# Performance work log

Measured on AMD Instinct MI355X. Metric: run time of the kernel, lower is better.

## Reference

```python
import jax, jax.numpy as jnp
from jax import lax
import numpy as np

# inferred ssconv semantics (custom CUDA kernel not in source):
#  - input x: (B, H, W, Cin) channels-last, Cin = per-pixel channel count
#  - in_index: (B, H, W) in [0, IN_GROUPS): routes each input pixel's Cin channels
#    to the corresponding slice of the weight's input-channel dim (gather/scatter MoE-style dispatch)
#  - weight: (OUT_GROUPS*Cout, IN_GROUPS*Cin, kh, kw), bias: (OUT_GROUPS*Cout,)
#  - per output pixel, one out-group is selected (maxout over groups); the kernel
#    returns both the selected Cout channels and the winning group index (out_index)

IN_GROUPS = 4
OUT_GROUPS = 4
STRIDE = 1  # pad = stride//2 in the wrapper; output (H-1)//s+1 == SAME padding


def setup_inputs() -> dict:
    key = jax.random.key(0)
    k1, k2, k3, k4 = jax.random.split(key, 4)
    x = jax.random.normal(k1, (8, 256, 256, 16), dtype=jnp.float32)
    in_index = jax.random.randint(k2, (8, 256, 256), 0, IN_GROUPS, dtype=jnp.int32)
    weight = jax.random.normal(k3, (64, 64, 3, 3), dtype=jnp.float32) * 0.05
    bias = jax.random.normal(k4, (64,), dtype=jnp.float32) * 0.05
    return {"x": x, "in_index": in_index, "weight": weight, "bias": bias}


def reference(x, in_index, weight, bias):
    B, H, W, Cin = x.shape
    OC, IC, kh, kw = weight.shape  # OC = OUT_GROUPS*Cout, IC = IN_GROUPS*Cin
    Cout = OC // OUT_GROUPS

    # dispatch: scatter each pixel's channels into its in-group slice (rest zero)
    onehot = jax.nn.one_hot(in_index, IN_GROUPS, dtype=x.dtype)          # (B,H,W,G)
    x_full = (onehot[..., :, None] * x[..., None, :]).reshape(B, H, W, IN_GROUPS * Cin)

    # dense conv over the dispatched tensor == per-pixel gathered group weights
    w_hwio = jnp.transpose(weight, (2, 3, 1, 0))  # (kh,kw,IC,OC)
    out = lax.conv_general_dilated(
        x_full, w_hwio, window_strides=(STRIDE, STRIDE), padding="SAME",
        dimension_numbers=("NHWC", "HWIO", "NHWC"))
    out = out + bias  # (B,H',W',OC)

    Bo, Ho, Wo, _ = out.shape
    out_g = out.reshape(Bo, Ho, Wo, OUT_GROUPS, Cout)
    scores = out_g.max(axis=-1)                    # (B,H',W',G) per-group response
    out_index = jnp.argmax(scores, axis=-1)        # winning out-group per pixel
    sel = jnp.take_along_axis(out_g, out_index[..., None, None], axis=3)
    sel = jnp.squeeze(sel, axis=3)                 # (B,H',W',Cout)
    return sel, out_index.astype(jnp.int32)
```

## Files before the change

kernel.cpp:

```cpp
#include <hip/hip_runtime.h>

#define H 256
#define W 256
#define BATCH 8
#define CIN 16
#define TW 32
#define TH 4
#define HWC (TW + 2)
#define HHC (TH + 2)
#define NHALO (HWC * HHC)
#define PXB 80
#define FIX_CAP 16384
#define GAP_TAU 2e-3f

#define OFF_XF   16384
#define XF_TERM  (NHALO * PXB)
#define OFF_SW   49024
#define OFF_BIAS 49280
#define OFF_RED  49536
#define SMEM_BYTES 49552

typedef __attribute__((ext_vector_type(4))) int i32x4;

__device__ __forceinline__ void gload_lds16(const void* g, void* l) {
    __builtin_amdgcn_global_load_lds(
        (const __attribute__((address_space(1))) unsigned int*)g,
        (__attribute__((address_space(3))) unsigned int*)l, 16, 0, 0);
}

template <int CTRL>
__device__ __forceinline__ float dpp_maxstep(float v) {
    int t = __builtin_amdgcn_update_dpp(0, __float_as_int(v), CTRL, 0xF, 0xF, true);
    return fmaxf(v, __int_as_float(t));
}
__device__ __forceinline__ float rowmax16(float v) {
    v = dpp_maxstep<0xB1>(v);
    v = dpp_maxstep<0x4E>(v);
    v = dpp_maxstep<0x124>(v);
    v = dpp_maxstep<0x128>(v);
    return v;
}

__global__ void wprep_kernel(const float* __restrict__ w, char* __restrict__ wt,
                             float* __restrict__ sw_ws, unsigned* __restrict__ fix_cnt) {
    const int n = blockIdx.x;
    const int k = threadIdx.x;
    if (n == 0 && k == 0) fix_cnt[0] = 0u;

    float v[9];
    float m = 0.f;
#pragma unroll
    for (int t = 0; t < 9; ++t) {
        v[t] = w[(n * 64 + k) * 9 + t];
        m = fmaxf(m, fabsf(v[t]));
    }
#pragma unroll
    for (int s = 1; s < 64; s <<= 1) m = fmaxf(m, __shfl_xor(m, s, 64));
    const float inv = (m > 0.f) ? (127.f / m) : 0.f;
    if (k == 0) sw_ws[n] = m * (1.f / 127.f);

    const int nt = n >> 4, nl = n & 15, kq = k >> 4, j = k & 15;
    const int lane16 = (kq * 16 + nl) * 16 + j;
#pragma unroll
    for (int t = 0; t < 9; ++t) {
        float f = v[t] * inv;
        int h = __float2int_rn(f);
        int l = __float2int_rn((f - (float)h) * 128.f);
        wt[((t * 2 + 0) * 4 + nt) * 1024 + lane16] = (char)h;
        wt[((t * 2 + 1) * 4 + nt) * 1024 + lane16] = (char)l;
    }
}

__global__ __launch_bounds__(256, 3) void ssconv_i8_kernel(
    const float* __restrict__ x, const int* __restrict__ gidx,
    const char* __restrict__ wt, const float* __restrict__ sw_ws,
    const float* __restrict__ bias,
    float* __restrict__ out_sel, float* __restrict__ out_idx,
    unsigned* __restrict__ fix_cnt, unsigned* __restrict__ fix_list)
{
    __shared__ __align__(16) char smem[SMEM_BYTES];
    char*  bufB  = smem;
    char*  xF    = smem + OFF_XF;
    float* swdL  = (float*)(smem + OFF_SW);
    float* biasL = (float*)(smem + OFF_BIAS);
    float* redL  = (float*)(smem + OFF_RED);

    const int tid  = threadIdx.x;
    const int x0   = blockIdx.x * TW;
    const int y0   = blockIdx.y * TH;
    const int bz   = blockIdx.z;
    const int wvid = tid >> 6;
    const int L    = tid & 63;
    const int q    = L >> 4;
    const int lm   = L & 15;

#pragma unroll
    for (int it = 0; it < 2; ++it) {
        int seg = it * 4 + wvid;
        gload_lds16(wt + seg * 1024 + L * 16, bufB + seg * 1024 + L * 16);
    }

    if (tid < 64) { swdL[tid] = sw_ws[tid]; biasL[tid] = bias[tid]; }

    float4 av0 = make_float4(0, 0, 0, 0), av1 = av0, av2 = av0, av3 = av0;
    int gv = 0;
    float am = 0.f;
    if (tid < NHALO) {
        int r = tid / HWC, c = tid - r * HWC;
        int hy = y0 + r - 1, hx = x0 + c - 1;
        if (hy >= 0 && hy < H && hx >= 0 && hx < W) {
            const float4* src = (const float4*)(x + (((size_t)bz * H + hy) * W + hx) * CIN);
            av0 = src[0]; av1 = src[1]; av2 = src[2]; av3 = src[3];
            gv = gidx[((size_t)bz * H + hy) * W + hx];
        }
        am = fmaxf(fmaxf(fmaxf(fabsf(av0.x), fabsf(av0.y)), fmaxf(fabsf(av0.z), fabsf(av0.w))),
              fmaxf(fmaxf(fmaxf(fabsf(av1.x), fabsf(av1.y)), fmaxf(fabsf(av1.z), fabsf(av1.w))),
              fmaxf(fmaxf(fmaxf(fabsf(av2.x), fabsf(av2.y)), fmaxf(fabsf(av2.z), fabsf(av2.w))),
                    fmaxf(fmaxf(fabsf(av3.x), fabsf(av3.y)), fmaxf(fabsf(av3.z), fabsf(av3.w))))));
    }
#pragma unroll
    for (int s = 1; s < 64; s <<= 1) am = fmaxf(am, __shfl_xor(am, s, 64));
    if (L == 0) redL[wvid] = am;
    __syncthreads();
    float bm = fmaxf(fmaxf(redL[0], redL[1]), fmaxf(redL[2], redL[3]));
    const float qinv = (bm > 0.f) ? (127.f / bm) : 0.f;
    const float sB   = bm * (1.f / 127.f);

    if (tid < NHALO) {
        float fs[16] = {av0.x, av0.y, av0.z, av0.w, av1.x, av1.y, av1.z, av1.w,
                        av2.x, av2.y, av2.z, av2.w, av3.x, av3.y, av3.z, av3.w};
        unsigned hw[4], lw[4];
#pragma unroll
        for (int j = 0; j < 4; ++j) {
            unsigned hword = 0, lword = 0;
#pragma unroll
            for (int e = 0; e < 4; ++e) {
                float f_ = fs[j * 4 + e] * qinv;
                int h_ = __float2int_rn(f_);
                int l_ = __float2int_rn((f_ - (float)h_) * 128.f);
                hword |= ((unsigned)(h_ & 255)) << (8 * e);
                lword |= ((unsigned)(l_ & 255)) << (8 * e);
            }
            hw[j] = hword; lw[j] = lword;
        }
        uint4 zz = make_uint4(0, 0, 0, 0);
        char* ph = xF + tid * PXB;
        char* pl = xF + XF_TERM + tid * PXB;
#pragma unroll
        for (int s = 0; s < 4; ++s) {
            *(uint4*)(ph + s * 16) = (s == gv) ? make_uint4(hw[0], hw[1], hw[2], hw[3]) : zz;
            *(uint4*)(pl + s * 16) = (s == gv) ? make_uint4(lw[0], lw[1], lw[2], lw[3]) : zz;
        }
    }
    __syncthreads();

    i32x4 acc1[2][4] = {};
    i32x4 acc2[2][4] = {};

#pragma unroll 1
    for (int tap = 0; tap < 9; ++tap) {
        if (tap < 8) {
            const char* gsrc = wt + (size_t)(tap + 1) * 8192;
            char* ldst = bufB + ((tap + 1) & 1) * 8192;
#pragma unroll
            for (int it = 0; it < 2; ++it) {
                int seg = it * 4 + wvid;
                gload_lds16(gsrc + seg * 1024 + L * 16, ldst + seg * 1024 + L * 16);
            }
        }

        const char* bB = bufB + (tap & 1) * 8192;
        const int dy = tap / 3, dx = tap - dy * 3;
        const int hbase = (wvid + dy) * HWC + lm + dx;

        i32x4 bh[4], bl[4];
#pragma unroll
        for (int nt = 0; nt < 4; ++nt) {
            bh[nt] = *(const i32x4*)(bB + nt * 1024 + L * 16);
            bl[nt] = *(const i32x4*)(bB + 4096 + nt * 1024 + L * 16);
        }
#pragma unroll
        for (int m = 0; m < 2; ++m) {
            const char* pA = xF + (hbase + 16 * m) * PXB + q * 16;
            i32x4 a0 = *(const i32x4*)pA;
            i32x4 a1 = *(const i32x4*)(pA + XF_TERM);
#pragma unroll
            for (int nt = 0; nt < 4; ++nt) {
                acc1[m][nt] = __builtin_amdgcn_mfma_i32_16x16x64_i8(a0, bh[nt], acc1[m][nt], 0, 0, 0);
                acc2[m][nt] = __builtin_amdgcn_mfma_i32_16x16x64_i8(a0, bl[nt], acc2[m][nt], 0, 0, 0);
                acc2[m][nt] = __builtin_amdgcn_mfma_i32_16x16x64_i8(a1, bh[nt], acc2[m][nt], 0, 0, 0);
            }
        }
        __syncthreads();
    }

    float swb[4], bsr[4];
#pragma unroll
    for (int nt = 0; nt < 4; ++nt) {
        swb[nt] = sB * swdL[nt * 16 + lm];
        bsr[nt] = biasL[nt * 16 + lm];
    }

    const int gy = y0 + wvid;
#pragma unroll
    for (int m = 0; m < 2; ++m) {
#pragma unroll
        for (int r = 0; r < 4; ++r) {
            float v0 = swb[0] * ((float)acc1[m][0][r] + (float)acc2[m][0][r] * (1.f / 128.f)) + bsr[0];
            float v1 = swb[1] * ((float)acc1[m][1][r] + (float)acc2[m][1][r] * (1.f / 128.f)) + bsr[1];
            float v2 = swb[2] * ((float)acc1[m][2][r] + (float)acc2[m][2][r] * (1.f / 128.f)) + bsr[2];
            float v3 = swb[3] * ((float)acc1[m][3][r] + (float)acc2[m][3][r] * (1.f / 128.f)) + bsr[3];

            float g0 = rowmax16(v0);
            float g1 = rowmax16(v1);
            float g2 = rowmax16(v2);
            float g3 = rowmax16(v3);
            int bg = 0; float best = g0;
            if (g1 > best) { best = g1; bg = 1; }
            if (g2 > best) { best = g2; bg = 2; }
            if (g3 > best) { best = g3; bg = 3; }

            float selv = (bg == 0) ? v0 : (bg == 1) ? v1 : (bg == 2) ? v2 : v3;

            const int gx = x0 + m * 16 + q * 4 + r;
            const size_t opix = ((size_t)bz * H + gy) * W + gx;
            out_sel[opix * 16 + lm] = selv;

            if (lm == 0) {
                out_idx[opix] = (float)bg;
                float o1v = (bg == 0) ? g1 : g0;
                float o2v = (bg <= 1) ? g2 : g1;
                float o3v = (bg <= 2) ? g3 : g2;
                float second = fmaxf(o1v, fmaxf(o2v, o3v));
                if (best - second < GAP_TAU) {
                    unsigned slot = atomicAdd(fix_cnt, 1u);
                    if (slot < FIX_CAP) fix_list[slot] = (unsigned)opix;
                }
            }
        }
    }
}

__global__ void fixup_kernel(const float* __restrict__ x, const int* __restrict__ gidx,
                             const float* __restrict__ w, const float* __restrict__ bias,
                             float* __restrict__ out_sel, float* __restrict__ out_idx,
                             const unsigned* __restrict__ fix_cnt,
                             const unsigned* __restrict__ fix_list)
{
    unsigned n = *fix_cnt;
    if (n > FIX_CAP) n = FIX_CAP;
    const int lane = threadIdx.x & 63;
    const int nwaves = gridDim.x * (blockDim.x >> 6);
    unsigned widx = blockIdx.x * (blockDim.x >> 6) + (threadIdx.x >> 6);

    for (; widx < n; widx += nwaves) {
        unsigned opix = fix_list[widx];
        int b  = opix >> 16;
        int y  = (opix >> 8) & 255;
        int xc = opix & 255;
        double acc = (double)bias[lane];
        for (int dy = 0; dy < 3; ++dy) {
            int yy = y + dy - 1;
            if (yy < 0 || yy >= H) continue;
            for (int dx = 0; dx < 3; ++dx) {
                int xx = xc + dx - 1;
                if (xx < 0 || xx >= W) continue;
                size_t pix = ((size_t)b * H + yy) * W + xx;
                int g = gidx[pix];
                const float* xp = x + pix * 16;
                const float* wp = w + (size_t)(lane * 64 + g * 16) * 9 + (dy * 3 + dx);
#pragma unroll
                for (int c = 0; c < 16; ++c)
                    acc = fma((double)wp[c * 9], (double)xp[c], acc);
            }
        }
        double m = acc;
        m = fmax(m, __shfl_xor(m, 1, 64));
        m = fmax(m, __shfl_xor(m, 2, 64));
        m = fmax(m, __shfl_xor(m, 4, 64));
        m = fmax(m, __shfl_xor(m, 8, 64));
        double g0 = __shfl(m, 0, 64), g1 = __shfl(m, 16, 64);
        double g2 = __shfl(m, 32, 64), g3 = __shfl(m, 48, 64);
        int bg = 0; double bb = g0;
        if (g1 > bb) { bb = g1; bg = 1; }
        if (g2 > bb) { bb = g2; bg = 2; }
        if (g3 > bb) { bb = g3; bg = 3; }
        if ((lane >> 4) == bg) out_sel[(size_t)opix * 16 + (lane & 15)] = (float)acc;
        if (lane == 0) out_idx[opix] = (float)bg;
    }
}

extern "C" void kernel_launch(void* const* d_in, const int* in_sizes, int n_in,
                              void* d_out, int out_size, void* d_ws, size_t ws_size,
                              hipStream_t stream) {
    const float* x    = (const float*)d_in[0];
    const int*   gidx = (const int*)d_in[1];
    const float* w    = (const float*)d_in[2];
    const float* bias = (const float*)d_in[3];

    char*     wt       = (char*)d_ws;
    float*    sw_ws    = (float*)((char*)d_ws + 73728);
    unsigned* fix_cnt  = (unsigned*)((char*)d_ws + 73984);
    unsigned* fix_list = (unsigned*)((char*)d_ws + 74000);

    float* out_sel = (float*)d_out;
    float* out_idx = (float*)d_out + (size_t)BATCH * H * W * CIN;

    wprep_kernel<<<64, 64, 0, stream>>>(w, wt, sw_ws, fix_cnt);

    dim3 grid(W / TW, H / TH, BATCH);
    ssconv_i8_kernel<<<grid, 256, 0, stream>>>(x, gidx, wt, sw_ws, bias,
                                               out_sel, out_idx, fix_cnt, fix_list);
    fixup_kernel<<<256, 256, 0, stream>>>(x, gidx, w, bias, out_sel, out_idx,
                                          fix_cnt, fix_list);
}
```

Before: 215.8 us.

## Replace split-int8 MFMA conv with fp16 MFMA and on-the-fly group masking

```diff
diff --git a/kernel.cpp b/kernel.cpp
--- a/kernel.cpp
+++ b/kernel.cpp
@@ -9,18 +9,23 @@
 #define HWC (TW + 2)
 #define HHC (TH + 2)
 #define NHALO (HWC * HHC)
-#define PXB 80
+#define PXA 40
 #define FIX_CAP 16384
-#define GAP_TAU 2e-3f
-
-#define OFF_XF   16384
-#define XF_TERM  (NHALO * PXB)
-#define OFF_SW   49024
-#define OFF_BIAS 49280
-#define OFF_RED  49536
-#define SMEM_BYTES 49552
-
-typedef __attribute__((ext_vector_type(4))) int i32x4;
+#define GAP_TAU 6e-3f
+
+#define OFF_XH   16384
+#define OFF_GS   24544
+#define OFF_BIAS 25360
+#define SMEM_BYTES 25616
+
+typedef __attribute__((ext_vector_type(8))) short short8;
+typedef __attribute__((ext_vector_type(8))) _Float16 half8;
+typedef __attribute__((ext_vector_type(4))) float f32x4;
+
+union S8H8 { short8 s; half8 h; };
+__device__ __forceinline__ half8 as_h8(short8 s) { S8H8 u; u.s = s; return u.h; }
+union HU { _Float16 h; unsigned short u; };
+__device__ __forceinline__ unsigned short f2h(float f) { HU u; u.h = (_Float16)f; return u.u; }
 
 __device__ __forceinline__ void gload_lds16(const void* g, void* l) {
     __builtin_amdgcn_global_load_lds(
@@ -41,49 +46,31 @@
     return v;
 }
 
-__global__ void wprep_kernel(const float* __restrict__ w, char* __restrict__ wt,
-                             float* __restrict__ sw_ws, unsigned* __restrict__ fix_cnt) {
+__global__ void wprep_kernel(const float* __restrict__ w, unsigned short* __restrict__ wt,
+                             unsigned* __restrict__ fix_cnt) {
     const int n = blockIdx.x;
     const int k = threadIdx.x;
     if (n == 0 && k == 0) fix_cnt[0] = 0u;
 
-    float v[9];
-    float m = 0.f;
-#pragma unroll
-    for (int t = 0; t < 9; ++t) {
-        v[t] = w[(n * 64 + k) * 9 + t];
-        m = fmaxf(m, fabsf(v[t]));
-    }
-#pragma unroll
-    for (int s = 1; s < 64; s <<= 1) m = fmaxf(m, __shfl_xor(m, s, 64));
-    const float inv = (m > 0.f) ? (127.f / m) : 0.f;
-    if (k == 0) sw_ws[n] = m * (1.f / 127.f);
-
-    const int nt = n >> 4, nl = n & 15, kq = k >> 4, j = k & 15;
-    const int lane16 = (kq * 16 + nl) * 16 + j;
-#pragma unroll
-    for (int t = 0; t < 9; ++t) {
-        float f = v[t] * inv;
-        int h = __float2int_rn(f);
-        int l = __float2int_rn((f - (float)h) * 128.f);
-        wt[((t * 2 + 0) * 4 + nt) * 1024 + lane16] = (char)h;
-        wt[((t * 2 + 1) * 4 + nt) * 1024 + lane16] = (char)l;
-    }
-}
-
-__global__ __launch_bounds__(256, 3) void ssconv_i8_kernel(
+    const int nt = n >> 4, lm = n & 15;
+    const int ks = k >> 5, q = (k >> 3) & 3, j = k & 7;
+    const int dst = ((0 * 2 + ks) * 4 + nt) * 512 + (q * 16 + lm) * 8 + j;
+#pragma unroll
+    for (int t = 0; t < 9; ++t)
+        wt[dst + t * 4096] = f2h(w[(n * 64 + k) * 9 + t] * 64.0f);
+}
+
+__global__ __launch_bounds__(256, 4) void ssconv_f16_kernel(
     const float* __restrict__ x, const int* __restrict__ gidx,
-    const char* __restrict__ wt, const float* __restrict__ sw_ws,
-    const float* __restrict__ bias,
+    const unsigned short* __restrict__ wt, const float* __restrict__ bias,
     float* __restrict__ out_sel, float* __restrict__ out_idx,
     unsigned* __restrict__ fix_cnt, unsigned* __restrict__ fix_list)
 {
     __shared__ __align__(16) char smem[SMEM_BYTES];
     char*  bufB  = smem;
-    char*  xF    = smem + OFF_XF;
-    float* swdL  = (float*)(smem + OFF_SW);
+    char*  xH    = smem + OFF_XH;
+    int*   gsL   = (int*)(smem + OFF_GS);
     float* biasL = (float*)(smem + OFF_BIAS);
-    float* redL  = (float*)(smem + OFF_RED);
 
     const int tid  = threadIdx.x;
     const int x0   = blockIdx.x * TW;
@@ -93,74 +80,43 @@
     const int L    = tid & 63;
     const int q    = L >> 4;
     const int lm   = L & 15;
+    const int c0   = (q & 1) * 8;
 
 #pragma unroll
     for (int it = 0; it < 2; ++it) {
         int seg = it * 4 + wvid;
-        gload_lds16(wt + seg * 1024 + L * 16, bufB + seg * 1024 + L * 16);
-    }
-
-    if (tid < 64) { swdL[tid] = sw_ws[tid]; biasL[tid] = bias[tid]; }
-
-    float4 av0 = make_float4(0, 0, 0, 0), av1 = av0, av2 = av0, av3 = av0;
-    int gv = 0;
-    float am = 0.f;
+        gload_lds16((const char*)wt + seg * 1024 + L * 16, bufB + seg * 1024 + L * 16);
+    }
+
+    if (tid < 64) biasL[tid] = bias[tid];
+
     if (tid < NHALO) {
         int r = tid / HWC, c = tid - r * HWC;
         int hy = y0 + r - 1, hx = x0 + c - 1;
+        float4 a0 = make_float4(0, 0, 0, 0), a1 = a0, a2 = a0, a3 = a0;
+        int g = 0;
         if (hy >= 0 && hy < H && hx >= 0 && hx < W) {
             const float4* src = (const float4*)(x + (((size_t)bz * H + hy) * W + hx) * CIN);
-            av0 = src[0]; av1 = src[1]; av2 = src[2]; av3 = src[3];
-            gv = gidx[((size_t)bz * H + hy) * W + hx];
-        }
-        am = fmaxf(fmaxf(fmaxf(fabsf(av0.x), fabsf(av0.y)), fmaxf(fabsf(av0.z), fabsf(av0.w))),
-              fmaxf(fmaxf(fmaxf(fabsf(av1.x), fabsf(av1.y)), fmaxf(fabsf(av1.z), fabsf(av1.w))),
-              fmaxf(fmaxf(fmaxf(fabsf(av2.x), fabsf(av2.y)), fmaxf(fabsf(av2.z), fabsf(av2.w))),
-                    fmaxf(fmaxf(fabsf(av3.x), fabsf(av3.y)), fmaxf(fabsf(av3.z), fabsf(av3.w))))));
-    }
-#pragma unroll
-    for (int s = 1; s < 64; s <<= 1) am = fmaxf(am, __shfl_xor(am, s, 64));
-    if (L == 0) redL[wvid] = am;
+            a0 = src[0]; a1 = src[1]; a2 = src[2]; a3 = src[3];
+            g = gidx[((size_t)bz * H + hy) * W + hx];
+        }
+        short8 v0, v1;
+        v0[0] = (short)f2h(a0.x); v0[1] = (short)f2h(a0.y); v0[2] = (short)f2h(a0.z); v0[3] = (short)f2h(a0.w);
+        v0[4] = (short)f2h(a1.x); v0[5] = (short)f2h(a1.y); v0[6] = (short)f2h(a1.z); v0[7] = (short)f2h(a1.w);
+        v1[0] = (short)f2h(a2.x); v1[1] = (short)f2h(a2.y); v1[2] = (short)f2h(a2.z); v1[3] = (short)f2h(a2.w);
+        v1[4] = (short)f2h(a3.x); v1[5] = (short)f2h(a3.y); v1[6] = (short)f2h(a3.z); v1[7] = (short)f2h(a3.w);
+        *(short8*)(xH + tid * PXA + 0)  = v0;
+        *(short8*)(xH + tid * PXA + 16) = v1;
+        gsL[tid] = g;
+    }
     __syncthreads();
-    float bm = fmaxf(fmaxf(redL[0], redL[1]), fmaxf(redL[2], redL[3]));
-    const float qinv = (bm > 0.f) ? (127.f / bm) : 0.f;
-    const float sB   = bm * (1.f / 127.f);
-
-    if (tid < NHALO) {
-        float fs[16] = {av0.x, av0.y, av0.z, av0.w, av1.x, av1.y, av1.z, av1.w,
-                        av2.x, av2.y, av2.z, av2.w, av3.x, av3.y, av3.z, av3.w};
-        unsigned hw[4], lw[4];
-#pragma unroll
-        for (int j = 0; j < 4; ++j) {
-            unsigned hword = 0, lword = 0;
-#pragma unroll
-            for (int e = 0; e < 4; ++e) {
-                float f_ = fs[j * 4 + e] * qinv;
-                int h_ = __float2int_rn(f_);
-                int l_ = __float2int_rn((f_ - (float)h_) * 128.f);
-                hword |= ((unsigned)(h_ & 255)) << (8 * e);
-                lword |= ((unsigned)(l_ & 255)) << (8 * e);
-            }
-            hw[j] = hword; lw[j] = lword;
-        }
-        uint4 zz = make_uint4(0, 0, 0, 0);
-        char* ph = xF + tid * PXB;
-        char* pl = xF + XF_TERM + tid * PXB;
-#pragma unroll
-        for (int s = 0; s < 4; ++s) {
-            *(uint4*)(ph + s * 16) = (s == gv) ? make_uint4(hw[0], hw[1], hw[2], hw[3]) : zz;
-            *(uint4*)(pl + s * 16) = (s == gv) ? make_uint4(lw[0], lw[1], lw[2], lw[3]) : zz;
-        }
-    }
-    __syncthreads();
-
-    i32x4 acc1[2][4] = {};
-    i32x4 acc2[2][4] = {};
+
+    f32x4 acc[2][4] = {};
 
 #pragma unroll 1
     for (int tap = 0; tap < 9; ++tap) {
         if (tap < 8) {
-            const char* gsrc = wt + (size_t)(tap + 1) * 8192;
+            const char* gsrc = (const char*)wt + (size_t)(tap + 1) * 8192;
             char* ldst = bufB + ((tap + 1) & 1) * 8192;
 #pragma unroll
             for (int it = 0; it < 2; ++it) {
@@ -173,43 +129,49 @@
         const int dy = tap / 3, dx = tap - dy * 3;
         const int hbase = (wvid + dy) * HWC + lm + dx;
 
-        i32x4 bh[4], bl[4];
-#pragma unroll
-        for (int nt = 0; nt < 4; ++nt) {
-            bh[nt] = *(const i32x4*)(bB + nt * 1024 + L * 16);
-            bl[nt] = *(const i32x4*)(bB + 4096 + nt * 1024 + L * 16);
-        }
+        int gg[2];
+        short8 ah[2];
 #pragma unroll
         for (int m = 0; m < 2; ++m) {
-            const char* pA = xF + (hbase + 16 * m) * PXB + q * 16;
-            i32x4 a0 = *(const i32x4*)pA;
-            i32x4 a1 = *(const i32x4*)(pA + XF_TERM);
-#pragma unroll
-            for (int nt = 0; nt < 4; ++nt) {
-                acc1[m][nt] = __builtin_amdgcn_mfma_i32_16x16x64_i8(a0, bh[nt], acc1[m][nt], 0, 0, 0);
-                acc2[m][nt] = __builtin_amdgcn_mfma_i32_16x16x64_i8(a0, bl[nt], acc2[m][nt], 0, 0, 0);
-                acc2[m][nt] = __builtin_amdgcn_mfma_i32_16x16x64_i8(a1, bh[nt], acc2[m][nt], 0, 0, 0);
+            int hb = hbase + 16 * m;
+            gg[m] = gsL[hb];
+            ah[m] = *(const short8*)(xH + hb * PXA + c0 * 2);
+        }
+
+        const short8 z = (short8)0;
+#pragma unroll
+        for (int ks = 0; ks < 2; ++ks) {
+            const int gk = ks * 2 + (q >> 1);
+            short8 bh[4];
+#pragma unroll
+            for (int nt = 0; nt < 4; ++nt)
+                bh[nt] = *(const short8*)(bB + (ks * 4 + nt) * 1024 + L * 16);
+#pragma unroll
+            for (int m = 0; m < 2; ++m) {
+                short8 a0 = (gg[m] == gk) ? ah[m] : z;
+#pragma unroll
+                for (int nt = 0; nt < 4; ++nt)
+                    acc[m][nt] = __builtin_amdgcn_mfma_f32_16x16x32_f16(
+                        as_h8(a0), as_h8(bh[nt]), acc[m][nt], 0, 0, 0);
             }
         }
         __syncthreads();
     }
 
-    float swb[4], bsr[4];
-#pragma unroll
-    for (int nt = 0; nt < 4; ++nt) {
-        swb[nt] = sB * swdL[nt * 16 + lm];
-        bsr[nt] = biasL[nt * 16 + lm];
-    }
-
+    float bsr[4];
+#pragma unroll
+    for (int nt = 0; nt < 4; ++nt) bsr[nt] = biasL[nt * 16 + lm];
+
+    const float SC = 0.015625f;
     const int gy = y0 + wvid;
 #pragma unroll
     for (int m = 0; m < 2; ++m) {
 #pragma unroll
         for (int r = 0; r < 4; ++r) {
-            float v0 = swb[0] * ((float)acc1[m][0][r] + (float)acc2[m][0][r] * (1.f / 128.f)) + bsr[0];
-            float v1 = swb[1] * ((float)acc1[m][1][r] + (float)acc2[m][1][r] * (1.f / 128.f)) + bsr[1];
-            float v2 = swb[2] * ((float)acc1[m][2][r] + (float)acc2[m][2][r] * (1.f / 128.f)) + bsr[2];
-            float v3 = swb[3] * ((float)acc1[m][3][r] + (float)acc2[m][3][r] * (1.f / 128.f)) + bsr[3];
+            float v0 = acc[m][0][r] * SC + bsr[0];
+            float v1 = acc[m][1][r] * SC + bsr[1];
+            float v2 = acc[m][2][r] * SC + bsr[2];
+            float v3 = acc[m][3][r] * SC + bsr[3];
 
             float g0 = rowmax16(v0);
             float g1 = rowmax16(v1);
@@ -298,19 +260,18 @@
     const float* w    = (const float*)d_in[2];
     const float* bias = (const float*)d_in[3];
 
-    char*     wt       = (char*)d_ws;
-    float*    sw_ws    = (float*)((char*)d_ws + 73728);
-    unsigned* fix_cnt  = (unsigned*)((char*)d_ws + 73984);
-    unsigned* fix_list = (unsigned*)((char*)d_ws + 74000);
+    unsigned short* wt = (unsigned short*)d_ws;
+    unsigned* fix_cnt  = (unsigned*)((char*)d_ws + 73728);
+    unsigned* fix_list = (unsigned*)((char*)d_ws + 73744);
 
     float* out_sel = (float*)d_out;
     float* out_idx = (float*)d_out + (size_t)BATCH * H * W * CIN;
 
-    wprep_kernel<<<64, 64, 0, stream>>>(w, wt, sw_ws, fix_cnt);
+    wprep_kernel<<<64, 64, 0, stream>>>(w, wt, fix_cnt);
 
     dim3 grid(W / TW, H / TH, BATCH);
-    ssconv_i8_kernel<<<grid, 256, 0, stream>>>(x, gidx, wt, sw_ws, bias,
-                                               out_sel, out_idx, fix_cnt, fix_list);
+    ssconv_f16_kernel<<<grid, 256, 0, stream>>>(x, gidx, wt, bias,
+                                                out_sel, out_idx, fix_cnt, fix_list);
     fixup_kernel<<<256, 256, 0, stream>>>(x, gidx, w, bias, out_sel, out_idx,
                                           fix_cnt, fix_list);
 }
```

Measured after the change: 375.4 us. 1.74x slower.
